# Kernel optimization log

Hardware: AMD Instinct MI355X
Metric: run time of the kernel (lower is better)

Reference implementation:

```python
import jax, jax.numpy as jnp
import numpy as np

N_NODES = 100000
N_EDGES = 600000
IN_DIM, HID_DIM, OUT_DIM = 128, 128, 128
NEG_SLOPE = 0.2  # PyG GATConv default


def _glorot(key, shape):
    fan = sum(shape)
    lim = jnp.sqrt(6.0 / fan)
    return jax.random.uniform(key, shape, jnp.float32, -lim, lim)


def setup_inputs() -> dict:
    key = jax.random.key(0)
    ks = jax.random.split(key, 10)
    x = jax.random.normal(ks[0], (N_NODES, IN_DIM), jnp.float32)
    edge_index = jax.random.randint(ks[1], (2, N_EDGES), 0, N_NODES, jnp.int64)
    return {
        "x": x,
        "edge_index": edge_index,
        "W1": _glorot(ks[2], (IN_DIM, HID_DIM)),
        "a_src1": _glorot(ks[3], (HID_DIM,)),
        "a_dst1": _glorot(ks[4], (HID_DIM,)),
        "b1": jnp.zeros((HID_DIM,), jnp.float32),
        "W2": _glorot(ks[5], (HID_DIM, OUT_DIM)),
        "a_src2": _glorot(ks[6], (OUT_DIM,)),
        "a_dst2": _glorot(ks[7], (OUT_DIM,)),
        "b2": jnp.zeros((OUT_DIM,), jnp.float32),
    }


def _gat_conv(x, src, dst, W, a_src, a_dst, b, n_nodes):
    """Single-head PyG-style GATConv (concat=True, heads=1, with self-loops already in src/dst)."""
    h = x @ W                                   # [N, F]
    alpha_s = h @ a_src                         # [N]
    alpha_d = h @ a_dst                         # [N]
    e = jax.nn.leaky_relu(alpha_s[src] + alpha_d[dst], NEG_SLOPE)  # [E]
    # segment softmax over incoming edges of each dst node
    m = jax.lax.stop_gradient(jax.ops.segment_max(e, dst, num_segments=n_nodes))
    w = jnp.exp(e - m[dst])                     # [E]
    denom = jax.ops.segment_sum(w, dst, num_segments=n_nodes)  # [N]
    alpha = w / denom[dst]                      # [E]
    out = jax.ops.segment_sum(h[src] * alpha[:, None], dst, num_segments=n_nodes)
    return out + b


def reference(x, edge_index, W1, a_src1, a_dst1, b1, W2, a_src2, a_dst2, b2):
    n = x.shape[0]
    loop = jnp.arange(n, dtype=edge_index.dtype)
    src = jnp.concatenate([edge_index[0], loop])  # add self-loops (PyG default)
    dst = jnp.concatenate([edge_index[1], loop])
    h = jax.nn.relu(_gat_conv(x, src, dst, W1, a_src1, a_dst1, b1, n))
    out = _gat_conv(h, src, dst, W2, a_src2, a_dst2, b2, n)
    return out.mean(axis=0)  # [out_dim]
```

## Files before the change

### kernel.cpp

```cpp
#include <hip/hip_runtime.h>


#define NEG_SLOPE 0.2f

typedef __attribute__((ext_vector_type(8))) short bf16x8;
typedef __attribute__((ext_vector_type(4))) float f32x4;

__device__ __forceinline__ float leaky(float x) { return x > 0.0f ? x : NEG_SLOPE * x; }

__device__ __forceinline__ unsigned int bf16rne(float f) {
  unsigned int u = __float_as_uint(f);
  return (u + 0x7fffu + ((u >> 16) & 1u)) >> 16;
}
__device__ __forceinline__ unsigned int packbf(float a, float b) {
  return bf16rne(a) | (bf16rne(b) << 16);
}
__device__ __forceinline__ float bf_lo(unsigned int u) { return __uint_as_float(u << 16); }
__device__ __forceinline__ float bf_hi(unsigned int u) { return __uint_as_float(u & 0xffff0000u); }

__device__ __forceinline__ void accum8(float* a, float w, uint4 h) {
  a[0] += w * bf_lo(h.x); a[1] += w * bf_hi(h.x);
  a[2] += w * bf_lo(h.y); a[3] += w * bf_hi(h.y);
  a[4] += w * bf_lo(h.z); a[5] += w * bf_hi(h.z);
  a[6] += w * bf_lo(h.w); a[7] += w * bf_hi(h.w);
}

__device__ __forceinline__ float gat_node_agg(const uint4* __restrict__ H4,
                                              const float* __restrict__ vas,
                                              const int* __restrict__ esrc,
                                              int s, int deg, float adv, float eself,
                                              uint4 hs, int lane, int l, float* acc) {
  float wself, dsum;
  if (deg <= 16) {
    const bool a = l < deg;
    int uj = 0;
    if (a) uj = esrc[s + l];
    float vsr = vas[uj];
    uint4 hb[8];
#pragma unroll
    for (int i = 0; i < 8; i++) {
      int ut = __shfl(uj, (lane & 48) + i, 64);
      hb[i] = H4[(size_t)ut * 16 + l];
    }
    const bool big = deg > 8;
    uint4 hc[8];
    if (big) {
#pragma unroll
      for (int i = 0; i < 8; i++) {
        int ut = __shfl(uj, (lane & 48) + 8 + i, 64);
        hc[i] = H4[(size_t)ut * 16 + l];
      }
    }
    float wj = a ? __expf(leaky(vsr + adv) - eself) : 0.f;
    wself = 1.0f;
    dsum = wj;
#pragma unroll
    for (int o = 8; o; o >>= 1) dsum += __shfl_xor(dsum, o, 16);
#pragma unroll
    for (int i = 0; i < 8; i++) {
      float w = __shfl(wj, (lane & 48) + i, 64);
      accum8(acc, w, hb[i]);
    }
    if (big) {
#pragma unroll
      for (int i = 0; i < 8; i++) {
        float w = __shfl(wj, (lane & 48) + 8 + i, 64);
        accum8(acc, w, hc[i]);
      }
    }
  } else {
    float m = eself;
    for (int t0 = 0; t0 < deg; t0 += 16) {
      int j = t0 + l;
      if (j < deg) m = fmaxf(m, leaky(vas[esrc[s + j]] + adv));
    }
#pragma unroll
    for (int o = 8; o; o >>= 1) m = fmaxf(m, __shfl_xor(m, o, 16));
    wself = __expf(eself - m);
    float dl = 0.f;
    for (int t0 = 0; t0 < deg; t0 += 16) {
      int j = t0 + l;
      int u2 = 0;
      float w2 = 0.f;
      if (j < deg) {
        u2 = esrc[s + j];
        w2 = __expf(leaky(vas[u2] + adv) - m);
        dl += w2;
      }
      const int cnt = min(16, deg - t0);
      for (int i0 = 0; i0 < cnt; i0 += 8) {
        const int tb = cnt - i0;
        uint4 hb[8];
        float wt[8];
#pragma unroll
        for (int i = 0; i < 8; i++) {
          if (i < tb) {
            int ut = __shfl(u2, (lane & 48) + i0 + i, 64);
            wt[i] = __shfl(w2, (lane & 48) + i0 + i, 64);
            hb[i] = H4[(size_t)ut * 16 + l];
          }
        }
#pragma unroll
        for (int i = 0; i < 8; i++)
          if (i < tb) accum8(acc, wt[i], hb[i]);
      }
    }
    dsum = dl;
#pragma unroll
    for (int o = 8; o; o >>= 1) dsum += __shfl_xor(dsum, o, 16);
  }
  accum8(acc, wself, hs);
  return 1.0f / (dsum + wself);
}

__global__ __launch_bounds__(256) void setup_k(const float* __restrict__ W1,
                                               const float* __restrict__ W2,
                                               unsigned short* __restrict__ Wf1,
                                               unsigned short* __restrict__ Wf2,
                                               int* __restrict__ deg,
                                               float* __restrict__ partial,
                                               int n, int nzb) {
  const int b = blockIdx.x;
  if (b < 2) {
    const float* W = b ? W2 : W1;
    unsigned short* Wf = b ? Wf2 : Wf1;
    for (int idx = threadIdx.x; idx < 16384; idx += 256) {
      int j = idx & 7;
      int lane = (idx >> 3) & 63;
      int fid = idx >> 9;
      int ct = fid >> 2, ks = fid & 3;
      int q = lane >> 4, l15 = lane & 15;
      Wf[idx] = (unsigned short)bf16rne(W[(ks * 32 + q * 8 + j) * 128 + ct * 16 + l15]);
    }
    return;
  }
  if (b == 2) {
    for (int i = threadIdx.x; i < 64 * 128; i += 256) partial[i] = 0.f;
    return;
  }
  int base = (b - 3) * 1024 + threadIdx.x * 4;
#pragma unroll
  for (int i = 0; i < 4; i++)
    if (base + i < n) deg[base + i] = 0;
}

__global__ void hist_kernel(const int* __restrict__ dst, int* __restrict__ deg, int E) {
  int e = blockIdx.x * 256 + threadIdx.x;
  if (e < E) atomicAdd(&deg[dst[e]], 1);
}

__global__ void scan_a(const int* __restrict__ cnt, int* __restrict__ exc,
                       int* __restrict__ bsum, int n) {
  __shared__ int sh[256];
  int b = blockIdx.x, tid = threadIdx.x;
  int base = b * 1024 + tid * 4;
  int v[4];
#pragma unroll
  for (int i = 0; i < 4; i++) v[i] = (base + i < n) ? cnt[base + i] : 0;
  int tsum = v[0] + v[1] + v[2] + v[3];
  sh[tid] = tsum;
  __syncthreads();
  for (int o = 1; o < 256; o <<= 1) {
    int t = (tid >= o) ? sh[tid - o] : 0;
    __syncthreads();
    sh[tid] += t;
    __syncthreads();
  }
  if (tid == 255) bsum[b] = sh[255];
  int run = sh[tid] - tsum;
#pragma unroll
  for (int i = 0; i < 4; i++) {
    if (base + i < n) exc[base + i] = run;
    run += v[i];
  }
}

__global__ void scan_c2(const int* __restrict__ exc, const int* __restrict__ bsum,
                        int* __restrict__ rowst, int* __restrict__ fill, int n, int E,
                        int nb) {
  __shared__ int red[256];
  int b = blockIdx.x, tid = threadIdx.x;
  red[tid] = (tid < b && tid < nb) ? bsum[tid] : 0;
  __syncthreads();
#pragma unroll
  for (int o = 128; o; o >>= 1) {
    if (tid < o) red[tid] += red[tid + o];
    __syncthreads();
  }
  int off = red[0];
  int base = b * 1024 + tid * 4;
#pragma unroll
  for (int i = 0; i < 4; i++) {
    int idx = base + i;
    if (idx < n) {
      int v = exc[idx] + off;
      rowst[idx] = v;
      fill[idx] = v;
    }
  }
  if (b == 0 && tid == 0) rowst[n] = E;
}

__global__ void scatter_kernel(const int* __restrict__ src, const int* __restrict__ dst,
                               int* __restrict__ fill, int* __restrict__ esrc, int E) {
  int e = blockIdx.x * 256 + threadIdx.x;
  if (e < E) {
    int v = dst[e];
    int p = atomicAdd(&fill[v], 1);
    esrc[p] = src[e];
  }
}

__device__ __forceinline__ void cvt_f32(const float4* raw, bf16x8* xf) {
#pragma unroll
  for (int ks = 0; ks < 4; ks++) {
    union { bf16x8 v; unsigned int u[4]; } cv;
    cv.u[0] = packbf(raw[2 * ks].x, raw[2 * ks].y);
    cv.u[1] = packbf(raw[2 * ks].z, raw[2 * ks].w);
    cv.u[2] = packbf(raw[2 * ks + 1].x, raw[2 * ks + 1].y);
    cv.u[3] = packbf(raw[2 * ks + 1].z, raw[2 * ks + 1].w);
    xf[ks] = cv.v;
  }
}

__device__ __forceinline__ void mfma_tile(const unsigned short* WL, const bf16x8* xf,
                                          const float* __restrict__ a_s,
                                          const float* __restrict__ a_d,
                                          unsigned short* __restrict__ H,
                                          float* __restrict__ vas,
                                          float* __restrict__ vad, int myrow, bool act,
                                          int lane, int q) {
  f32x4 acc[8];
#pragma unroll
  for (int ct = 0; ct < 8; ct++) acc[ct] = (f32x4){0.f, 0.f, 0.f, 0.f};
#pragma unroll
  for (int ks = 0; ks < 4; ks++) {
    bf16x8 wf[8];
#pragma unroll
    for (int ct = 0; ct < 8; ct++)
      wf[ct] = *(const bf16x8*)&WL[(((ct << 2) + ks) << 9) + lane * 8];
#pragma unroll
    for (int ct = 0; ct < 8; ct++)
      acc[ct] = __builtin_amdgcn_mfma_f32_16x16x32_bf16(wf[ct], xf[ks], acc[ct], 0, 0, 0);
  }
  float ds = 0.f, dd = 0.f;
#pragma unroll
  for (int ct = 0; ct < 8; ct++) {
    const int c0 = ct * 16 + q * 4;
    float4 as4 = *(const float4*)&a_s[c0];
    float4 ad4 = *(const float4*)&a_d[c0];
    ds += acc[ct][0] * as4.x + acc[ct][1] * as4.y + acc[ct][2] * as4.z + acc[ct][3] * as4.w;
    dd += acc[ct][0] * ad4.x + acc[ct][1] * ad4.y + acc[ct][2] * ad4.z + acc[ct][3] * ad4.w;
    if (act) {
      uint2 o;
      o.x = packbf(acc[ct][0], acc[ct][1]);
      o.y = packbf(acc[ct][2], acc[ct][3]);
      *(uint2*)&H[(size_t)myrow * 128 + c0] = o;
    }
  }
  ds += __shfl_xor(ds, 16, 64);
  ds += __shfl_xor(ds, 32, 64);
  dd += __shfl_xor(dd, 16, 64);
  dd += __shfl_xor(dd, 32, 64);
  if (q == 0 && act) {
    vas[myrow] = ds;
    vad[myrow] = dd;
  }
}

__global__ __launch_bounds__(256) void gemm_mfma1(const float* __restrict__ Xf,
                                                  const unsigned short* __restrict__ Wf,
                                                  const float* __restrict__ a_s,
                                                  const float* __restrict__ a_d,
                                                  unsigned short* __restrict__ H,
                                                  float* __restrict__ vas,
                                                  float* __restrict__ vad, int n,
                                                  int nt16, int ngemm) {
  __shared__ unsigned short WL[32 * 512];
  const int lane = threadIdx.x & 63;
  const int wv = threadIdx.x >> 6;
  const int l15 = lane & 15;
  const int q = lane >> 4;
  const int t0 = blockIdx.x * 4 + wv;
  const int t1 = t0 + ngemm * 4;
  const int r0 = t0 * 16 + l15;
  const int r1 = t1 * 16 + l15;
  const bool wact0 = t0 < nt16;
  const bool wact1 = t1 < nt16;
  const bool act0 = wact0 && (r0 < n);
  const bool act1 = wact1 && (r1 < n);

  float4 raw0[8];
  if (wact0) {
#pragma unroll
    for (int ks = 0; ks < 4; ks++) {
      float4 z = {0.f, 0.f, 0.f, 0.f};
      raw0[2 * ks] = z;
      raw0[2 * ks + 1] = z;
      if (act0) {
        raw0[2 * ks] = *(const float4*)&Xf[(size_t)r0 * 128 + ks * 32 + q * 8];
        raw0[2 * ks + 1] = *(const float4*)&Xf[(size_t)r0 * 128 + ks * 32 + q * 8 + 4];
      }
    }
  }
  {
    const uint4* __restrict__ Wg4 = (const uint4*)Wf;
    uint4* WL4 = (uint4*)WL;
#pragma unroll
    for (int j = 0; j < 8; j++) WL4[threadIdx.x + 256 * j] = Wg4[threadIdx.x + 256 * j];
  }
  __syncthreads();
  if (!wact0) return;

  float4 raw1[8];
  if (wact1) {
#pragma unroll
    for (int ks = 0; ks < 4; ks++) {
      float4 z = {0.f, 0.f, 0.f, 0.f};
      raw1[2 * ks] = z;
      raw1[2 * ks + 1] = z;
      if (act1) {
        raw1[2 * ks] = *(const float4*)&Xf[(size_t)r1 * 128 + ks * 32 + q * 8];
        raw1[2 * ks + 1] = *(const float4*)&Xf[(size_t)r1 * 128 + ks * 32 + q * 8 + 4];
      }
    }
  }

  bf16x8 xf[4];
  cvt_f32(raw0, xf);
  mfma_tile(WL, xf, a_s, a_d, H, vas, vad, r0, act0, lane, q);
  if (wact1) {
    cvt_f32(raw1, xf);
    mfma_tile(WL, xf, a_s, a_d, H, vas, vad, r1, act1, lane, q);
  }
}

__global__ __launch_bounds__(256, 4) void agg1_gemm2(
    const unsigned short* __restrict__ HA, const float* __restrict__ vas1,
    const float* __restrict__ vad1, const int* __restrict__ rowst,
    const int* __restrict__ esrc, const float* __restrict__ b1,
    const unsigned short* __restrict__ Wf2, const float* __restrict__ a_s2,
    const float* __restrict__ a_d2, unsigned short* __restrict__ HB,
    float* __restrict__ vas2, float* __restrict__ vad2, int n) {
  __shared__ unsigned short Atile[16 * 128];
  __shared__ float sdot[2][4][16];
  const int tid = threadIdx.x;
  const int lane = tid & 63;
  const int wv = tid >> 6;
  const int q = lane >> 4;
  const int l = lane & 15;
  const int row = wv * 4 + q;
  const int node = blockIdx.x * 16 + row;
  const uint4* __restrict__ H4 = (const uint4*)HA;

  float acc[8];
#pragma unroll
  for (int k = 0; k < 8; k++) acc[k] = 0.f;

  uint4 o = {0u, 0u, 0u, 0u};
  if (node < n) {
    const int s = rowst[node];
    const int deg = rowst[node + 1] - s;
    const float adv = vad1[node];
    const float eself = leaky(vas1[node] + adv);
    uint4 hs = H4[(size_t)node * 16 + l];
    const float inv = gat_node_agg(H4, vas1, esrc, s, deg, adv, eself, hs, lane, l, acc);

    float4 b0 = *(const float4*)&b1[8 * l];
    float4 b1v = *(const float4*)&b1[8 * l + 4];
    acc[0] = fmaxf(acc[0] * inv + b0.x, 0.f);
    acc[1] = fmaxf(acc[1] * inv + b0.y, 0.f);
    acc[2] = fmaxf(acc[2] * inv + b0.z, 0.f);
    acc[3] = fmaxf(acc[3] * inv + b0.w, 0.f);
    acc[4] = fmaxf(acc[4] * inv + b1v.x, 0.f);
    acc[5] = fmaxf(acc[5] * inv + b1v.y, 0.f);
    acc[6] = fmaxf(acc[6] * inv + b1v.z, 0.f);
    acc[7] = fmaxf(acc[7] * inv + b1v.w, 0.f);
    o.x = packbf(acc[0], acc[1]);
    o.y = packbf(acc[2], acc[3]);
    o.z = packbf(acc[4], acc[5]);
    o.w = packbf(acc[6], acc[7]);
  }
  *(uint4*)&Atile[row * 128 + ((l ^ (row & 7)) << 3)] = o;
  __syncthreads();

  bf16x8 xf[4];
#pragma unroll
  for (int ks = 0; ks < 4; ks++)
    xf[ks] = *(const bf16x8*)&Atile[l * 128 + ((((ks << 2) + q) ^ (l & 7)) << 3)];

  const int ct0 = 2 * wv, ct1 = 2 * wv + 1;
  f32x4 accA = {0.f, 0.f, 0.f, 0.f}, accB = {0.f, 0.f, 0.f, 0.f};
#pragma unroll
  for (int ks = 0; ks < 4; ks++) {
    bf16x8 w0 = *(const bf16x8*)&Wf2[(((ct0 << 2) + ks) << 9) + lane * 8];
    bf16x8 w1 = *(const bf16x8*)&Wf2[(((ct1 << 2) + ks) << 9) + lane * 8];
    accA = __builtin_amdgcn_mfma_f32_16x16x32_bf16(w0, xf[ks], accA, 0, 0, 0);
    accB = __builtin_amdgcn_mfma_f32_16x16x32_bf16(w1, xf[ks], accB, 0, 0, 0);
  }

  const int myrow = blockIdx.x * 16 + l;
  const bool ract = myrow < n;
  float ds = 0.f, dd = 0.f;
  {
    const int c0 = ct0 * 16 + q * 4;
    float4 as4 = *(const float4*)&a_s2[c0];
    float4 ad4 = *(const float4*)&a_d2[c0];
    ds += accA[0] * as4.x + accA[1] * as4.y + accA[2] * as4.z + accA[3] * as4.w;
    dd += accA[0] * ad4.x + accA[1] * ad4.y + accA[2] * ad4.z + accA[3] * ad4.w;
    if (ract) {
      uint2 ov;
      ov.x = packbf(accA[0], accA[1]);
      ov.y = packbf(accA[2], accA[3]);
      *(uint2*)&HB[(size_t)myrow * 128 + c0] = ov;
    }
  }
  {
    const int c0 = ct1 * 16 + q * 4;
    float4 as4 = *(const float4*)&a_s2[c0];
    float4 ad4 = *(const float4*)&a_d2[c0];
    ds += accB[0] * as4.x + accB[1] * as4.y + accB[2] * as4.z + accB[3] * as4.w;
    dd += accB[0] * ad4.x + accB[1] * ad4.y + accB[2] * ad4.z + accB[3] * ad4.w;
    if (ract) {
      uint2 ov;
      ov.x = packbf(accB[0], accB[1]);
      ov.y = packbf(accB[2], accB[3]);
      *(uint2*)&HB[(size_t)myrow * 128 + c0] = ov;
    }
  }
  ds += __shfl_xor(ds, 16, 64);
  ds += __shfl_xor(ds, 32, 64);
  dd += __shfl_xor(dd, 16, 64);
  dd += __shfl_xor(dd, 32, 64);
  if (q == 0) {
    sdot[0][wv][l] = ds;
    sdot[1][wv][l] = dd;
  }
  __syncthreads();
  if (tid < 16) {
    int nn = blockIdx.x * 16 + tid;
    if (nn < n) {
      vas2[nn] = sdot[0][0][tid] + sdot[0][1][tid] + sdot[0][2][tid] + sdot[0][3][tid];
      vad2[nn] = sdot[1][0][tid] + sdot[1][1][tid] + sdot[1][2][tid] + sdot[1][3][tid];
    }
  }
}

__global__ __launch_bounds__(256, 4) void gat_agg_l2(const unsigned short* __restrict__ H,
                                                     const float* __restrict__ vas,
                                                     const float* __restrict__ vad,
                                                     const int* __restrict__ rowst,
                                                     const int* __restrict__ esrc,
                                                     const float* __restrict__ bias,
                                                     float* __restrict__ partial, int n) {
  const int tid = threadIdx.x;
  const int lane = tid & 63;
  const int wv = tid >> 6;
  const int q = lane >> 4;
  const int l = lane & 15;
  const int node = (blockIdx.x * 4 + wv) * 4 + q;
  const uint4* __restrict__ H4 = (const uint4*)H;

  float acc[8];
#pragma unroll
  for (int k = 0; k < 8; k++) acc[k] = 0.f;

  if (node < n) {
    const int s = rowst[node];
    const int deg = rowst[node + 1] - s;
    const float adv = vad[node];
    const float eself = leaky(vas[node] + adv);
    uint4 hs = H4[(size_t)node * 16 + l];
    const float inv = gat_node_agg(H4, vas, esrc, s, deg, adv, eself, hs, lane, l, acc);

    float4 b0 = *(const float4*)&bias[8 * l];
    float4 b1v = *(const float4*)&bias[8 * l + 4];
    acc[0] = acc[0] * inv + b0.x; acc[1] = acc[1] * inv + b0.y;
    acc[2] = acc[2] * inv + b0.z; acc[3] = acc[3] * inv + b0.w;
    acc[4] = acc[4] * inv + b1v.x; acc[5] = acc[5] * inv + b1v.y;
    acc[6] = acc[6] * inv + b1v.z; acc[7] = acc[7] * inv + b1v.w;
  }

#pragma unroll
  for (int k = 0; k < 8; k++) {
    acc[k] += __shfl_xor(acc[k], 16, 64);
    acc[k] += __shfl_xor(acc[k], 32, 64);
  }
  __shared__ float red[4][128];
  if (q == 0) {
#pragma unroll
    for (int k = 0; k < 8; k++) red[wv][8 * l + k] = acc[k];
  }
  __syncthreads();
  if (tid < 128) {
    float sm = red[0][tid] + red[1][tid] + red[2][tid] + red[3][tid];
    atomicAdd(&partial[(blockIdx.x & 63) * 128 + tid], sm);
  }
}

__global__ void finalize_k(const float* __restrict__ partial, float* __restrict__ out,
                           float invn) {
  int c = threadIdx.x;
  float s = 0.f;
#pragma unroll 8
  for (int r = 0; r < 64; r++) s += partial[r * 128 + c];
  out[c] = s * invn;
}

extern "C" void kernel_launch(void* const* d_in, const int* in_sizes, int n_in,
                              void* d_out, int out_size, void* d_ws, size_t ws_size,
                              hipStream_t stream) {
  const float* x = (const float*)d_in[0];
  const int* ei = (const int*)d_in[1];
  const float* W1 = (const float*)d_in[2];
  const float* a_src1 = (const float*)d_in[3];
  const float* a_dst1 = (const float*)d_in[4];
  const float* b1 = (const float*)d_in[5];
  const float* W2 = (const float*)d_in[6];
  const float* a_src2 = (const float*)d_in[7];
  const float* a_dst2 = (const float*)d_in[8];
  const float* b2 = (const float*)d_in[9];
  float* out = (float*)d_out;

  const int N = in_sizes[0] / 128;
  const int E = in_sizes[1] / 2;
  const int* src = ei;
  const int* dst = ei + E;

  const size_t rowpadded = (size_t)(N + 256) * 128;

  char* p = (char*)d_ws;
  unsigned short* HA = (unsigned short*)p; p += rowpadded * 2;
  unsigned short* HB = (unsigned short*)p; p += rowpadded * 2;
  float* vas1 = (float*)p;    p += (size_t)N * 4;
  float* vad1 = (float*)p;    p += (size_t)N * 4;
  float* vas2 = (float*)p;    p += (size_t)N * 4;
  float* vad2 = (float*)p;    p += (size_t)N * 4;
  int* deg = (int*)p;         p += (size_t)N * 4;
  int* rowst = (int*)p;       p += (size_t)(N + 1) * 4;
  int* fill = (int*)p;        p += (size_t)N * 4;
  int* esrc = (int*)p;        p += (size_t)E * 4;
  int* exc = (int*)p;         p += (size_t)N * 4;
  int* bsum = (int*)p;        p += 256 * 4;
  float* partial = (float*)p; p += 64 * 128 * 4;
  unsigned short* Wf1 = (unsigned short*)p; p += 16384 * 2;
  unsigned short* Wf2 = (unsigned short*)p; p += 16384 * 2;

  const int nb = (N + 1023) / 1024;
  const int eblocks = (E + 255) / 256;
  const int nt16 = (N + 15) / 16;
  const int ngemm = (nt16 + 7) / 8;
  const int aggblocks = (N + 15) / 16;

  setup_k<<<3 + nb, 256, 0, stream>>>(W1, W2, Wf1, Wf2, deg, partial, N, nb);
  hist_kernel<<<eblocks, 256, 0, stream>>>(dst, deg, E);
  scan_a<<<nb, 256, 0, stream>>>(deg, exc, bsum, N);
  scan_c2<<<nb, 256, 0, stream>>>(exc, bsum, rowst, fill, N, E, nb);
  scatter_kernel<<<eblocks, 256, 0, stream>>>(src, dst, fill, esrc, E);
  gemm_mfma1<<<ngemm, 256, 0, stream>>>(x, Wf1, a_src1, a_dst1, HA, vas1, vad1, N, nt16, ngemm);
  agg1_gemm2<<<aggblocks, 256, 0, stream>>>(HA, vas1, vad1, rowst, esrc, b1, Wf2,
                                            a_src2, a_dst2, HB, vas2, vad2, N);
  gat_agg_l2<<<aggblocks, 256, 0, stream>>>(HB, vas2, vad2, rowst, esrc, b2, partial, N);
  finalize_k<<<1, 128, 0, stream>>>(partial, out, 1.0f / (float)N);
}
```

Before: 267.7 us.

## Add padded per-node 16-slot neighbor table to cut dependent loads in aggregation

```diff
diff --git a/kernel.cpp b/kernel.cpp
--- a/kernel.cpp
+++ b/kernel.cpp
@@ -27,27 +27,32 @@
 
 __device__ __forceinline__ float gat_node_agg(const uint4* __restrict__ H4,
                                               const float* __restrict__ vas,
+                                              const int* __restrict__ dega,
+                                              const int* __restrict__ esrcp,
+                                              const int* __restrict__ rowst,
                                               const int* __restrict__ esrc,
-                                              int s, int deg, float adv, float eself,
-                                              uint4 hs, int lane, int l, float* acc) {
+                                              int node, int nclamp, float adv,
+                                              float eself, uint4 hs, int lane, int l,
+                                              float* acc) {
+  int traw = esrcp[(size_t)node * 16 + l];
+  int dg = dega[node];
+  int ujc = min(max(traw, 0), nclamp);
+  float vsr = vas[ujc];
+  uint4 hb[8];
+#pragma unroll
+  for (int i = 0; i < 8; i++) {
+    int ut = __shfl(ujc, (lane & 48) + i, 64);
+    hb[i] = H4[(size_t)ut * 16 + l];
+  }
   float wself, dsum;
-  if (deg <= 16) {
-    const bool a = l < deg;
-    int uj = 0;
-    if (a) uj = esrc[s + l];
-    float vsr = vas[uj];
-    uint4 hb[8];
-#pragma unroll
-    for (int i = 0; i < 8; i++) {
-      int ut = __shfl(uj, (lane & 48) + i, 64);
-      hb[i] = H4[(size_t)ut * 16 + l];
-    }
-    const bool big = deg > 8;
+  if (dg <= 16) {
+    const bool a = l < dg;
+    const bool big = dg > 8;
     uint4 hc[8];
     if (big) {
 #pragma unroll
       for (int i = 0; i < 8; i++) {
-        int ut = __shfl(uj, (lane & 48) + 8 + i, 64);
+        int ut = __shfl(ujc, (lane & 48) + 8 + i, 64);
         hc[i] = H4[(size_t)ut * 16 + l];
       }
     }
@@ -69,6 +74,8 @@
       }
     }
   } else {
+    const int s = rowst[node];
+    const int deg = dg;
     float m = eself;
     for (int t0 = 0; t0 < deg; t0 += 16) {
       int j = t0 + l;
@@ -90,19 +97,19 @@
       const int cnt = min(16, deg - t0);
       for (int i0 = 0; i0 < cnt; i0 += 8) {
         const int tb = cnt - i0;
-        uint4 hb[8];
+        uint4 h2[8];
         float wt[8];
 #pragma unroll
         for (int i = 0; i < 8; i++) {
           if (i < tb) {
             int ut = __shfl(u2, (lane & 48) + i0 + i, 64);
             wt[i] = __shfl(w2, (lane & 48) + i0 + i, 64);
-            hb[i] = H4[(size_t)ut * 16 + l];
+            h2[i] = H4[(size_t)ut * 16 + l];
           }
         }
 #pragma unroll
         for (int i = 0; i < 8; i++)
-          if (i < tb) accum8(acc, wt[i], hb[i]);
+          if (i < tb) accum8(acc, wt[i], h2[i]);
       }
     }
     dsum = dl;
@@ -202,12 +209,16 @@
 }
 
 __global__ void scatter_kernel(const int* __restrict__ src, const int* __restrict__ dst,
-                               int* __restrict__ fill, int* __restrict__ esrc, int E) {
+                               int* __restrict__ fill, const int* __restrict__ rowst,
+                               int* __restrict__ esrc, int* __restrict__ esrcp, int E) {
   int e = blockIdx.x * 256 + threadIdx.x;
   if (e < E) {
     int v = dst[e];
+    int sv = src[e];
     int p = atomicAdd(&fill[v], 1);
-    esrc[p] = src[e];
+    esrc[p] = sv;
+    int p2 = p - rowst[v];
+    if (p2 < 16) esrcp[(size_t)v * 16 + p2] = sv;
   }
 }
 
@@ -337,7 +348,8 @@
 
 __global__ __launch_bounds__(256, 4) void agg1_gemm2(
     const unsigned short* __restrict__ HA, const float* __restrict__ vas1,
-    const float* __restrict__ vad1, const int* __restrict__ rowst,
+    const float* __restrict__ vad1, const int* __restrict__ dega,
+    const int* __restrict__ esrcp, const int* __restrict__ rowst,
     const int* __restrict__ esrc, const float* __restrict__ b1,
     const unsigned short* __restrict__ Wf2, const float* __restrict__ a_s2,
     const float* __restrict__ a_d2, unsigned short* __restrict__ HB,
@@ -359,12 +371,12 @@
 
   uint4 o = {0u, 0u, 0u, 0u};
   if (node < n) {
-    const int s = rowst[node];
-    const int deg = rowst[node + 1] - s;
     const float adv = vad1[node];
-    const float eself = leaky(vas1[node] + adv);
+    const float vsn = vas1[node];
     uint4 hs = H4[(size_t)node * 16 + l];
-    const float inv = gat_node_agg(H4, vas1, esrc, s, deg, adv, eself, hs, lane, l, acc);
+    const float eself = leaky(vsn + adv);
+    const float inv = gat_node_agg(H4, vas1, dega, esrcp, rowst, esrc, node, n - 1,
+                                   adv, eself, hs, lane, l, acc);
 
     float4 b0 = *(const float4*)&b1[8 * l];
     float4 b1v = *(const float4*)&b1[8 * l + 4];
@@ -449,6 +461,8 @@
 __global__ __launch_bounds__(256, 4) void gat_agg_l2(const unsigned short* __restrict__ H,
                                                      const float* __restrict__ vas,
                                                      const float* __restrict__ vad,
+                                                     const int* __restrict__ dega,
+                                                     const int* __restrict__ esrcp,
                                                      const int* __restrict__ rowst,
                                                      const int* __restrict__ esrc,
                                                      const float* __restrict__ bias,
@@ -466,12 +480,12 @@
   for (int k = 0; k < 8; k++) acc[k] = 0.f;
 
   if (node < n) {
-    const int s = rowst[node];
-    const int deg = rowst[node + 1] - s;
     const float adv = vad[node];
-    const float eself = leaky(vas[node] + adv);
+    const float vsn = vas[node];
     uint4 hs = H4[(size_t)node * 16 + l];
-    const float inv = gat_node_agg(H4, vas, esrc, s, deg, adv, eself, hs, lane, l, acc);
+    const float eself = leaky(vsn + adv);
+    const float inv = gat_node_agg(H4, vas, dega, esrcp, rowst, esrc, node, n - 1,
+                                   adv, eself, hs, lane, l, acc);
 
     float4 b0 = *(const float4*)&bias[8 * l];
     float4 b1v = *(const float4*)&bias[8 * l + 4];
@@ -540,6 +554,7 @@
   int* rowst = (int*)p;       p += (size_t)(N + 1) * 4;
   int* fill = (int*)p;        p += (size_t)N * 4;
   int* esrc = (int*)p;        p += (size_t)E * 4;
+  int* esrcp = (int*)p;       p += (size_t)N * 16 * 4;
   int* exc = (int*)p;         p += (size_t)N * 4;
   int* bsum = (int*)p;        p += 256 * 4;
   float* partial = (float*)p; p += 64 * 128 * 4;
@@ -556,10 +571,11 @@
   hist_kernel<<<eblocks, 256, 0, stream>>>(dst, deg, E);
   scan_a<<<nb, 256, 0, stream>>>(deg, exc, bsum, N);
   scan_c2<<<nb, 256, 0, stream>>>(exc, bsum, rowst, fill, N, E, nb);
-  scatter_kernel<<<eblocks, 256, 0, stream>>>(src, dst, fill, esrc, E);
+  scatter_kernel<<<eblocks, 256, 0, stream>>>(src, dst, fill, rowst, esrc, esrcp, E);
   gemm_mfma1<<<ngemm, 256, 0, stream>>>(x, Wf1, a_src1, a_dst1, HA, vas1, vad1, N, nt16, ngemm);
-  agg1_gemm2<<<aggblocks, 256, 0, stream>>>(HA, vas1, vad1, rowst, esrc, b1, Wf2,
-                                            a_src2, a_dst2, HB, vas2, vad2, N);
-  gat_agg_l2<<<aggblocks, 256, 0, stream>>>(HB, vas2, vad2, rowst, esrc, b2, partial, N);
+  agg1_gemm2<<<aggblocks, 256, 0, stream>>>(HA, vas1, vad1, deg, esrcp, rowst, esrc, b1,
+                                            Wf2, a_src2, a_dst2, HB, vas2, vad2, N);
+  gat_agg_l2<<<aggblocks, 256, 0, stream>>>(HB, vas2, vad2, deg, esrcp, rowst, esrc, b2,
+                                            partial, N);
   finalize_k<<<1, 128, 0, stream>>>(partial, out, 1.0f / (float)N);
 }
```

Result: no change. 270.6 us (+1.1%).

## Replace CSR build with padded 16-slot adjacency plus overflow list, two nodes per group

Applied to the files above, without the earlier changes.

```diff
diff --git a/kernel.cpp b/kernel.cpp
--- a/kernel.cpp
+++ b/kernel.cpp
@@ -25,101 +25,116 @@
   a[6] += w * bf_lo(h.w); a[7] += w * bf_hi(h.w);
 }
 
-__device__ __forceinline__ float gat_node_agg(const uint4* __restrict__ H4,
-                                              const float* __restrict__ vas,
-                                              const int* __restrict__ esrc,
-                                              int s, int deg, float adv, float eself,
-                                              uint4 hs, int lane, int l, float* acc) {
-  float wself, dsum;
-  if (deg <= 16) {
-    const bool a = l < deg;
-    int uj = 0;
-    if (a) uj = esrc[s + l];
-    float vsr = vas[uj];
-    uint4 hb[8];
+__device__ __forceinline__ float2 gat_node2(
+    const uint4* __restrict__ H4, const float* __restrict__ vas,
+    const float* __restrict__ vad, const int* __restrict__ fill,
+    const int* __restrict__ esrcp, const int2* __restrict__ ovf,
+    const int* __restrict__ ovfn, int node0, int node1, int nclamp,
+    int lane, int l, float* acc0, float* acc1, float* eself_out) {
+  int t0 = esrcp[(size_t)node0 * 16 + l];
+  int t1 = esrcp[(size_t)node1 * 16 + l];
+  int dg0 = fill[node0];
+  int dg1 = fill[node1];
+  float ad0 = vad[node0], ad1 = vad[node1];
+  float as0 = vas[node0], as1 = vas[node1];
+  uint4 hs0 = H4[(size_t)node0 * 16 + l];
+  uint4 hs1 = H4[(size_t)node1 * 16 + l];
+  int u0 = min(max(t0, 0), nclamp);
+  int u1 = min(max(t1, 0), nclamp);
+  float vs0 = vas[u0];
+  float vs1 = vas[u1];
+  uint4 hb0[8], hb1[8];
+#pragma unroll
+  for (int i = 0; i < 8; i++) {
+    int ut = __shfl(u0, (lane & 48) + i, 64);
+    hb0[i] = H4[(size_t)ut * 16 + l];
+  }
+#pragma unroll
+  for (int i = 0; i < 8; i++) {
+    int ut = __shfl(u1, (lane & 48) + i, 64);
+    hb1[i] = H4[(size_t)ut * 16 + l];
+  }
+  const bool big0 = dg0 > 8, big1 = dg1 > 8;
+  uint4 hc0[8];
+  if (big0) {
 #pragma unroll
     for (int i = 0; i < 8; i++) {
-      int ut = __shfl(uj, (lane & 48) + i, 64);
-      hb[i] = H4[(size_t)ut * 16 + l];
-    }
-    const bool big = deg > 8;
-    uint4 hc[8];
-    if (big) {
-#pragma unroll
-      for (int i = 0; i < 8; i++) {
-        int ut = __shfl(uj, (lane & 48) + 8 + i, 64);
-        hc[i] = H4[(size_t)ut * 16 + l];
+      int ut = __shfl(u0, (lane & 48) + 8 + i, 64);
+      hc0[i] = H4[(size_t)ut * 16 + l];
+    }
+  }
+  float es0 = leaky(as0 + ad0), es1 = leaky(as1 + ad1);
+  float wj0 = (l < dg0) ? __expf(leaky(vs0 + ad0) - es0) : 0.f;
+  float wj1 = (l < dg1) ? __expf(leaky(vs1 + ad1) - es1) : 0.f;
+  float ds0 = wj0, ds1 = wj1;
+#pragma unroll
+  for (int o = 8; o; o >>= 1) ds0 += __shfl_xor(ds0, o, 16);
+#pragma unroll
+  for (int o = 8; o; o >>= 1) ds1 += __shfl_xor(ds1, o, 16);
+#pragma unroll
+  for (int i = 0; i < 8; i++) {
+    float w = __shfl(wj0, (lane & 48) + i, 64);
+    accum8(acc0, w, hb0[i]);
+  }
+  if (big0) {
+#pragma unroll
+    for (int i = 0; i < 8; i++) {
+      float w = __shfl(wj0, (lane & 48) + 8 + i, 64);
+      accum8(acc0, w, hc0[i]);
+    }
+  }
+  uint4 hc1[8];
+  if (big1) {
+#pragma unroll
+    for (int i = 0; i < 8; i++) {
+      int ut = __shfl(u1, (lane & 48) + 8 + i, 64);
+      hc1[i] = H4[(size_t)ut * 16 + l];
+    }
+  }
+#pragma unroll
+  for (int i = 0; i < 8; i++) {
+    float w = __shfl(wj1, (lane & 48) + i, 64);
+    accum8(acc1, w, hb1[i]);
+  }
+  if (big1) {
+#pragma unroll
+    for (int i = 0; i < 8; i++) {
+      float w = __shfl(wj1, (lane & 48) + 8 + i, 64);
+      accum8(acc1, w, hc1[i]);
+    }
+  }
+  if (dg0 > 16 || dg1 > 16) {
+    int ovn = *ovfn;
+    for (int k = 0; k < ovn; k++) {
+      int2 ent = ovf[k];
+      if (ent.x == node0) {
+        float w = __expf(leaky(vas[ent.y] + ad0) - es0);
+        ds0 += w;
+        accum8(acc0, w, H4[(size_t)ent.y * 16 + l]);
       }
-    }
-    float wj = a ? __expf(leaky(vsr + adv) - eself) : 0.f;
-    wself = 1.0f;
-    dsum = wj;
-#pragma unroll
-    for (int o = 8; o; o >>= 1) dsum += __shfl_xor(dsum, o, 16);
-#pragma unroll
-    for (int i = 0; i < 8; i++) {
-      float w = __shfl(wj, (lane & 48) + i, 64);
-      accum8(acc, w, hb[i]);
-    }
-    if (big) {
-#pragma unroll
-      for (int i = 0; i < 8; i++) {
-        float w = __shfl(wj, (lane & 48) + 8 + i, 64);
-        accum8(acc, w, hc[i]);
+      if (ent.x == node1) {
+        float w = __expf(leaky(vas[ent.y] + ad1) - es1);
+        ds1 += w;
+        accum8(acc1, w, H4[(size_t)ent.y * 16 + l]);
       }
     }
-  } else {
-    float m = eself;
-    for (int t0 = 0; t0 < deg; t0 += 16) {
-      int j = t0 + l;
-      if (j < deg) m = fmaxf(m, leaky(vas[esrc[s + j]] + adv));
-    }
-#pragma unroll
-    for (int o = 8; o; o >>= 1) m = fmaxf(m, __shfl_xor(m, o, 16));
-    wself = __expf(eself - m);
-    float dl = 0.f;
-    for (int t0 = 0; t0 < deg; t0 += 16) {
-      int j = t0 + l;
-      int u2 = 0;
-      float w2 = 0.f;
-      if (j < deg) {
-        u2 = esrc[s + j];
-        w2 = __expf(leaky(vas[u2] + adv) - m);
-        dl += w2;
-      }
-      const int cnt = min(16, deg - t0);
-      for (int i0 = 0; i0 < cnt; i0 += 8) {
-        const int tb = cnt - i0;
-        uint4 hb[8];
-        float wt[8];
-#pragma unroll
-        for (int i = 0; i < 8; i++) {
-          if (i < tb) {
-            int ut = __shfl(u2, (lane & 48) + i0 + i, 64);
-            wt[i] = __shfl(w2, (lane & 48) + i0 + i, 64);
-            hb[i] = H4[(size_t)ut * 16 + l];
-          }
-        }
-#pragma unroll
-        for (int i = 0; i < 8; i++)
-          if (i < tb) accum8(acc, wt[i], hb[i]);
-      }
-    }
-    dsum = dl;
-#pragma unroll
-    for (int o = 8; o; o >>= 1) dsum += __shfl_xor(dsum, o, 16);
-  }
-  accum8(acc, wself, hs);
-  return 1.0f / (dsum + wself);
+  }
+  accum8(acc0, 1.0f, hs0);
+  accum8(acc1, 1.0f, hs1);
+  eself_out[0] = es0;
+  eself_out[1] = es1;
+  return make_float2(1.0f / (ds0 + 1.0f), 1.0f / (ds1 + 1.0f));
 }
 
 __global__ __launch_bounds__(256) void setup_k(const float* __restrict__ W1,
                                                const float* __restrict__ W2,
                                                unsigned short* __restrict__ Wf1,
                                                unsigned short* __restrict__ Wf2,
-                                               int* __restrict__ deg,
+                                               int* __restrict__ fill,
+                                               int* __restrict__ esrcp,
+                                               int* __restrict__ ovfn,
                                                float* __restrict__ partial,
-                                               int n, int nzb) {
+                                               int n, int nfb) {
   const int b = blockIdx.x;
   if (b < 2) {
     const float* W = b ? W2 : W1;
@@ -136,78 +151,39 @@
   }
   if (b == 2) {
     for (int i = threadIdx.x; i < 64 * 128; i += 256) partial[i] = 0.f;
+    if (threadIdx.x == 0) *ovfn = 0;
     return;
   }
-  int base = (b - 3) * 1024 + threadIdx.x * 4;
-#pragma unroll
-  for (int i = 0; i < 4; i++)
-    if (base + i < n) deg[base + i] = 0;
-}
-
-__global__ void hist_kernel(const int* __restrict__ dst, int* __restrict__ deg, int E) {
-  int e = blockIdx.x * 256 + threadIdx.x;
-  if (e < E) atomicAdd(&deg[dst[e]], 1);
-}
-
-__global__ void scan_a(const int* __restrict__ cnt, int* __restrict__ exc,
-                       int* __restrict__ bsum, int n) {
-  __shared__ int sh[256];
-  int b = blockIdx.x, tid = threadIdx.x;
-  int base = b * 1024 + tid * 4;
-  int v[4];
-#pragma unroll
-  for (int i = 0; i < 4; i++) v[i] = (base + i < n) ? cnt[base + i] : 0;
-  int tsum = v[0] + v[1] + v[2] + v[3];
-  sh[tid] = tsum;
-  __syncthreads();
-  for (int o = 1; o < 256; o <<= 1) {
-    int t = (tid >= o) ? sh[tid - o] : 0;
-    __syncthreads();
-    sh[tid] += t;
-    __syncthreads();
-  }
-  if (tid == 255) bsum[b] = sh[255];
-  int run = sh[tid] - tsum;
-#pragma unroll
-  for (int i = 0; i < 4; i++) {
-    if (base + i < n) exc[base + i] = run;
-    run += v[i];
-  }
-}
-
-__global__ void scan_c2(const int* __restrict__ exc, const int* __restrict__ bsum,
-                        int* __restrict__ rowst, int* __restrict__ fill, int n, int E,
-                        int nb) {
-  __shared__ int red[256];
-  int b = blockIdx.x, tid = threadIdx.x;
-  red[tid] = (tid < b && tid < nb) ? bsum[tid] : 0;
-  __syncthreads();
-#pragma unroll
-  for (int o = 128; o; o >>= 1) {
-    if (tid < o) red[tid] += red[tid + o];
-    __syncthreads();
-  }
-  int off = red[0];
-  int base = b * 1024 + tid * 4;
-#pragma unroll
-  for (int i = 0; i < 4; i++) {
-    int idx = base + i;
-    if (idx < n) {
-      int v = exc[idx] + off;
-      rowst[idx] = v;
-      fill[idx] = v;
-    }
-  }
-  if (b == 0 && tid == 0) rowst[n] = E;
+  if (b < 3 + nfb) {
+    int base = (b - 3) * 1024 + threadIdx.x * 4;
+#pragma unroll
+    for (int i = 0; i < 4; i++)
+      if (base + i < n) fill[base + i] = 0;
+    return;
+  }
+  size_t base = (size_t)(b - 3 - nfb) * 1024 + threadIdx.x * 4;
+  size_t tot = (size_t)n * 16;
+  if (base + 4 <= tot) {
+    *(int4*)&esrcp[base] = make_int4(0, 0, 0, 0);
+  } else {
+    for (size_t i = base; i < tot; i++) esrcp[i] = 0;
+  }
 }
 
 __global__ void scatter_kernel(const int* __restrict__ src, const int* __restrict__ dst,
-                               int* __restrict__ fill, int* __restrict__ esrc, int E) {
+                               int* __restrict__ fill, int* __restrict__ esrcp,
+                               int2* __restrict__ ovf, int* __restrict__ ovfn, int E) {
   int e = blockIdx.x * 256 + threadIdx.x;
   if (e < E) {
     int v = dst[e];
+    int sv = src[e];
     int p = atomicAdd(&fill[v], 1);
-    esrc[p] = src[e];
+    if (p < 16) {
+      esrcp[(size_t)v * 16 + p] = sv;
+    } else {
+      int k = atomicAdd(ovfn, 1);
+      ovf[k] = make_int2(v, sv);
+    }
   }
 }
 
@@ -335,161 +311,178 @@
   }
 }
 
-__global__ __launch_bounds__(256, 4) void agg1_gemm2(
+__global__ __launch_bounds__(256, 3) void agg1_gemm2(
     const unsigned short* __restrict__ HA, const float* __restrict__ vas1,
-    const float* __restrict__ vad1, const int* __restrict__ rowst,
-    const int* __restrict__ esrc, const float* __restrict__ b1,
+    const float* __restrict__ vad1, const int* __restrict__ fill,
+    const int* __restrict__ esrcp, const int2* __restrict__ ovf,
+    const int* __restrict__ ovfn, const float* __restrict__ b1,
     const unsigned short* __restrict__ Wf2, const float* __restrict__ a_s2,
     const float* __restrict__ a_d2, unsigned short* __restrict__ HB,
     float* __restrict__ vas2, float* __restrict__ vad2, int n) {
-  __shared__ unsigned short Atile[16 * 128];
-  __shared__ float sdot[2][4][16];
+  __shared__ unsigned short Atile[32 * 128];
+  __shared__ float sdot[2][2][4][16];
   const int tid = threadIdx.x;
   const int lane = tid & 63;
   const int wv = tid >> 6;
   const int q = lane >> 4;
   const int l = lane & 15;
   const int row = wv * 4 + q;
-  const int node = blockIdx.x * 16 + row;
+  const int base = blockIdx.x * 32;
+  const int node0 = base + row;
+  const int node1 = base + row + 16;
+  const bool valid0 = node0 < n, valid1 = node1 < n;
+  const int n0s = valid0 ? node0 : n - 1;
+  const int n1s = valid1 ? node1 : n - 1;
   const uint4* __restrict__ H4 = (const uint4*)HA;
 
-  float acc[8];
-#pragma unroll
-  for (int k = 0; k < 8; k++) acc[k] = 0.f;
-
-  uint4 o = {0u, 0u, 0u, 0u};
-  if (node < n) {
-    const int s = rowst[node];
-    const int deg = rowst[node + 1] - s;
-    const float adv = vad1[node];
-    const float eself = leaky(vas1[node] + adv);
-    uint4 hs = H4[(size_t)node * 16 + l];
-    const float inv = gat_node_agg(H4, vas1, esrc, s, deg, adv, eself, hs, lane, l, acc);
-
-    float4 b0 = *(const float4*)&b1[8 * l];
-    float4 b1v = *(const float4*)&b1[8 * l + 4];
-    acc[0] = fmaxf(acc[0] * inv + b0.x, 0.f);
-    acc[1] = fmaxf(acc[1] * inv + b0.y, 0.f);
-    acc[2] = fmaxf(acc[2] * inv + b0.z, 0.f);
-    acc[3] = fmaxf(acc[3] * inv + b0.w, 0.f);
-    acc[4] = fmaxf(acc[4] * inv + b1v.x, 0.f);
-    acc[5] = fmaxf(acc[5] * inv + b1v.y, 0.f);
-    acc[6] = fmaxf(acc[6] * inv + b1v.z, 0.f);
-    acc[7] = fmaxf(acc[7] * inv + b1v.w, 0.f);
-    o.x = packbf(acc[0], acc[1]);
-    o.y = packbf(acc[2], acc[3]);
-    o.z = packbf(acc[4], acc[5]);
-    o.w = packbf(acc[6], acc[7]);
-  }
-  *(uint4*)&Atile[row * 128 + ((l ^ (row & 7)) << 3)] = o;
+  float acc0[8], acc1[8];
+#pragma unroll
+  for (int k = 0; k < 8; k++) { acc0[k] = 0.f; acc1[k] = 0.f; }
+  float es[2];
+  float2 inv = gat_node2(H4, vas1, vad1, fill, esrcp, ovf, ovfn, n0s, n1s, n - 1,
+                         lane, l, acc0, acc1, es);
+
+  float4 b0 = *(const float4*)&b1[8 * l];
+  float4 b1v = *(const float4*)&b1[8 * l + 4];
+  uint4 o0 = {0u, 0u, 0u, 0u}, o1 = {0u, 0u, 0u, 0u};
+  if (valid0) {
+    float r0_ = fmaxf(acc0[0] * inv.x + b0.x, 0.f), r1_ = fmaxf(acc0[1] * inv.x + b0.y, 0.f);
+    float r2_ = fmaxf(acc0[2] * inv.x + b0.z, 0.f), r3_ = fmaxf(acc0[3] * inv.x + b0.w, 0.f);
+    float r4_ = fmaxf(acc0[4] * inv.x + b1v.x, 0.f), r5_ = fmaxf(acc0[5] * inv.x + b1v.y, 0.f);
+    float r6_ = fmaxf(acc0[6] * inv.x + b1v.z, 0.f), r7_ = fmaxf(acc0[7] * inv.x + b1v.w, 0.f);
+    o0.x = packbf(r0_, r1_); o0.y = packbf(r2_, r3_);
+    o0.z = packbf(r4_, r5_); o0.w = packbf(r6_, r7_);
+  }
+  if (valid1) {
+    float r0_ = fmaxf(acc1[0] * inv.y + b0.x, 0.f), r1_ = fmaxf(acc1[1] * inv.y + b0.y, 0.f);
+    float r2_ = fmaxf(acc1[2] * inv.y + b0.z, 0.f), r3_ = fmaxf(acc1[3] * inv.y + b0.w, 0.f);
+    float r4_ = fmaxf(acc1[4] * inv.y + b1v.x, 0.f), r5_ = fmaxf(acc1[5] * inv.y + b1v.y, 0.f);
+    float r6_ = fmaxf(acc1[6] * inv.y + b1v.z, 0.f), r7_ = fmaxf(acc1[7] * inv.y + b1v.w, 0.f);
+    o1.x = packbf(r0_, r1_); o1.y = packbf(r2_, r3_);
+    o1.z = packbf(r4_, r5_); o1.w = packbf(r6_, r7_);
+  }
+  *(uint4*)&Atile[row * 128 + ((l ^ (row & 7)) << 3)] = o0;
+  *(uint4*)&Atile[(row + 16) * 128 + ((l ^ (row & 7)) << 3)] = o1;
   __syncthreads();
 
-  bf16x8 xf[4];
-#pragma unroll
-  for (int ks = 0; ks < 4; ks++)
-    xf[ks] = *(const bf16x8*)&Atile[l * 128 + ((((ks << 2) + q) ^ (l & 7)) << 3)];
-
   const int ct0 = 2 * wv, ct1 = 2 * wv + 1;
-  f32x4 accA = {0.f, 0.f, 0.f, 0.f}, accB = {0.f, 0.f, 0.f, 0.f};
+  f32x4 aA0 = {0.f, 0.f, 0.f, 0.f}, aB0 = aA0, aA1 = aA0, aB1 = aA0;
 #pragma unroll
   for (int ks = 0; ks < 4; ks++) {
     bf16x8 w0 = *(const bf16x8*)&Wf2[(((ct0 << 2) + ks) << 9) + lane * 8];
     bf16x8 w1 = *(const bf16x8*)&Wf2[(((ct1 << 2) + ks) << 9) + lane * 8];
-    accA = __builtin_amdgcn_mfma_f32_16x16x32_bf16(w0, xf[ks], accA, 0, 0, 0);
-    accB = __builtin_amdgcn_mfma_f32_16x16x32_bf16(w1, xf[ks], accB, 0, 0, 0);
-  }
-
-  const int myrow = blockIdx.x * 16 + l;
-  const bool ract = myrow < n;
-  float ds = 0.f, dd = 0.f;
-  {
-    const int c0 = ct0 * 16 + q * 4;
-    float4 as4 = *(const float4*)&a_s2[c0];
-    float4 ad4 = *(const float4*)&a_d2[c0];
-    ds += accA[0] * as4.x + accA[1] * as4.y + accA[2] * as4.z + accA[3] * as4.w;
-    dd += accA[0] * ad4.x + accA[1] * ad4.y + accA[2] * ad4.z + accA[3] * ad4.w;
-    if (ract) {
-      uint2 ov;
-      ov.x = packbf(accA[0], accA[1]);
-      ov.y = packbf(accA[2], accA[3]);
-      *(uint2*)&HB[(size_t)myrow * 128 + c0] = ov;
-    }
-  }
-  {
-    const int c0 = ct1 * 16 + q * 4;
-    float4 as4 = *(const float4*)&a_s2[c0];
-    float4 ad4 = *(const float4*)&a_d2[c0];
-    ds += accB[0] * as4.x + accB[1] * as4.y + accB[2] * as4.z + accB[3] * as4.w;
-    dd += accB[0] * ad4.x + accB[1] * ad4.y + accB[2] * ad4.z + accB[3] * ad4.w;
-    if (ract) {
-      uint2 ov;
-      ov.x = packbf(accB[0], accB[1]);
-      ov.y = packbf(accB[2], accB[3]);
-      *(uint2*)&HB[(size_t)myrow * 128 + c0] = ov;
-    }
-  }
-  ds += __shfl_xor(ds, 16, 64);
-  ds += __shfl_xor(ds, 32, 64);
-  dd += __shfl_xor(dd, 16, 64);
-  dd += __shfl_xor(dd, 32, 64);
-  if (q == 0) {
-    sdot[0][wv][l] = ds;
-    sdot[1][wv][l] = dd;
+    bf16x8 x0 = *(const bf16x8*)&Atile[l * 128 + ((((ks << 2) + q) ^ (l & 7)) << 3)];
+    bf16x8 x1 = *(const bf16x8*)&Atile[(16 + l) * 128 + ((((ks << 2) + q) ^ (l & 7)) << 3)];
+    aA0 = __builtin_amdgcn_mfma_f32_16x16x32_bf16(w0, x0, aA0, 0, 0, 0);
+    aB0 = __builtin_amdgcn_mfma_f32_16x16x32_bf16(w1, x0, aB0, 0, 0, 0);
+    aA1 = __builtin_amdgcn_mfma_f32_16x16x32_bf16(w0, x1, aA1, 0, 0, 0);
+    aB1 = __builtin_amdgcn_mfma_f32_16x16x32_bf16(w1, x1, aB1, 0, 0, 0);
+  }
+
+#pragma unroll
+  for (int t = 0; t < 2; t++) {
+    f32x4 aA = t ? aA1 : aA0;
+    f32x4 aB = t ? aB1 : aB0;
+    const int myrow = base + t * 16 + l;
+    const bool ract = myrow < n;
+    float ds = 0.f, dd = 0.f;
+    {
+      const int c0 = ct0 * 16 + q * 4;
+      float4 as4 = *(const float4*)&a_s2[c0];
+      float4 ad4 = *(const float4*)&a_d2[c0];
+      ds += aA[0] * as4.x + aA[1] * as4.y + aA[2] * as4.z + aA[3] * as4.w;
+      dd += aA[0] * ad4.x + aA[1] * ad4.y + aA[2] * ad4.z + aA[3] * ad4.w;
+      if (ract) {
+        uint2 ov;
+        ov.x = packbf(aA[0], aA[1]);
+        ov.y = packbf(aA[2], aA[3]);
+        *(uint2*)&HB[(size_t)myrow * 128 + c0] = ov;
+      }
+    }
+    {
+      const int c0 = ct1 * 16 + q * 4;
+      float4 as4 = *(const float4*)&a_s2[c0];
+      float4 ad4 = *(const float4*)&a_d2[c0];
+      ds += aB[0] * as4.x + aB[1] * as4.y + aB[2] * as4.z + aB[3] * as4.w;
+      dd += aB[0] * ad4.x + aB[1] * ad4.y + aB[2] * ad4.z + aB[3] * ad4.w;
+      if (ract) {
+        uint2 ov;
+        ov.x = packbf(aB[0], aB[1]);
+        ov.y = packbf(aB[2], aB[3]);
+        *(uint2*)&HB[(size_t)myrow * 128 + c0] = ov;
+      }
+    }
+    ds += __shfl_xor(ds, 16, 64);
+    ds += __shfl_xor(ds, 32, 64);
+    dd += __shfl_xor(dd, 16, 64);
+    dd += __shfl_xor(dd, 32, 64);
+    if (q == 0) {
+      sdot[t][0][wv][l] = ds;
+      sdot[t][1][wv][l] = dd;
+    }
   }
   __syncthreads();
-  if (tid < 16) {
-    int nn = blockIdx.x * 16 + tid;
+  if (tid < 32) {
+    int t = tid >> 4, i = tid & 15;
+    int nn = base + tid;
     if (nn < n) {
-      vas2[nn] = sdot[0][0][tid] + sdot[0][1][tid] + sdot[0][2][tid] + sdot[0][3][tid];
-      vad2[nn] = sdot[1][0][tid] + sdot[1][1][tid] + sdot[1][2][tid] + sdot[1][3][tid];
-    }
-  }
-}
-
-__global__ __launch_bounds__(256, 4) void gat_agg_l2(const unsigned short* __restrict__ H,
-                                                     const float* __restrict__ vas,
-                                                     const float* __restrict__ vad,
-                                                     const int* __restrict__ rowst,
-                                                     const int* __restrict__ esrc,
-                                                     const float* __restrict__ bias,
-                                                     float* __restrict__ partial, int n) {
+      vas2[nn] = sdot[t][0][0][i] + sdot[t][0][1][i] + sdot[t][0][2][i] + sdot[t][0][3][i];
+      vad2[nn] = sdot[t][1][0][i] + sdot[t][1][1][i] + sdot[t][1][2][i] + sdot[t][1][3][i];
+    }
+  }
+}
+
+__global__ __launch_bounds__(256, 3) void gat_agg_l2(
+    const unsigned short* __restrict__ H, const float* __restrict__ vas,
+    const float* __restrict__ vad, const int* __restrict__ fill,
+    const int* __restrict__ esrcp, const int2* __restrict__ ovf,
+    const int* __restrict__ ovfn, const float* __restrict__ bias,
+    float* __restrict__ partial, int n) {
   const int tid = threadIdx.x;
   const int lane = tid & 63;
   const int wv = tid >> 6;
   const int q = lane >> 4;
   const int l = lane & 15;
-  const int node = (blockIdx.x * 4 + wv) * 4 + q;
+  const int row = wv * 4 + q;
+  const int base = blockIdx.x * 32;
+  const int node0 = base + row;
+  const int node1 = base + row + 16;
+  const bool valid0 = node0 < n, valid1 = node1 < n;
+  const int n0s = valid0 ? node0 : n - 1;
+  const int n1s = valid1 ? node1 : n - 1;
   const uint4* __restrict__ H4 = (const uint4*)H;
 
-  float acc[8];
-#pragma unroll
-  for (int k = 0; k < 8; k++) acc[k] = 0.f;
-
-  if (node < n) {
-    const int s = rowst[node];
-    const int deg = rowst[node + 1] - s;
-    const float adv = vad[node];
-    const float eself = leaky(vas[node] + adv);
-    uint4 hs = H4[(size_t)node * 16 + l];
-    const float inv = gat_node_agg(H4, vas, esrc, s, deg, adv, eself, hs, lane, l, acc);
-
-    float4 b0 = *(const float4*)&bias[8 * l];
-    float4 b1v = *(const float4*)&bias[8 * l + 4];
-    acc[0] = acc[0] * inv + b0.x; acc[1] = acc[1] * inv + b0.y;
-    acc[2] = acc[2] * inv + b0.z; acc[3] = acc[3] * inv + b0.w;
-    acc[4] = acc[4] * inv + b1v.x; acc[5] = acc[5] * inv + b1v.y;
-    acc[6] = acc[6] * inv + b1v.z; acc[7] = acc[7] * inv + b1v.w;
-  }
+  float acc0[8], acc1[8];
+#pragma unroll
+  for (int k = 0; k < 8; k++) { acc0[k] = 0.f; acc1[k] = 0.f; }
+  float es[2];
+  float2 inv = gat_node2(H4, vas, vad, fill, esrcp, ovf, ovfn, n0s, n1s, n - 1,
+                         lane, l, acc0, acc1, es);
+
+  float4 b0 = *(const float4*)&bias[8 * l];
+  float4 b1v = *(const float4*)&bias[8 * l + 4];
+  float out[8];
+  const float i0 = valid0 ? inv.x : 0.f;
+  const float i1 = valid1 ? inv.y : 0.f;
+  const float bm = (valid0 ? 1.f : 0.f) + (valid1 ? 1.f : 0.f);
+  out[0] = acc0[0] * i0 + acc1[0] * i1 + bm * b0.x;
+  out[1] = acc0[1] * i0 + acc1[1] * i1 + bm * b0.y;
+  out[2] = acc0[2] * i0 + acc1[2] * i1 + bm * b0.z;
+  out[3] = acc0[3] * i0 + acc1[3] * i1 + bm * b0.w;
+  out[4] = acc0[4] * i0 + acc1[4] * i1 + bm * b1v.x;
+  out[5] = acc0[5] * i0 + acc1[5] * i1 + bm * b1v.y;
+  out[6] = acc0[6] * i0 + acc1[6] * i1 + bm * b1v.z;
+  out[7] = acc0[7] * i0 + acc1[7] * i1 + bm * b1v.w;
 
 #pragma unroll
   for (int k = 0; k < 8; k++) {
-    acc[k] += __shfl_xor(acc[k], 16, 64);
-    acc[k] += __shfl_xor(acc[k], 32, 64);
+    out[k] += __shfl_xor(out[k], 16, 64);
+    out[k] += __shfl_xor(out[k], 32, 64);
   }
   __shared__ float red[4][128];
   if (q == 0) {
 #pragma unroll
-    for (int k = 0; k < 8; k++) red[wv][8 * l + k] = acc[k];
+    for (int k = 0; k < 8; k++) red[wv][8 * l + k] = out[k];
   }
   __syncthreads();
   if (tid < 128) {
@@ -536,30 +529,28 @@
   float* vad1 = (float*)p;    p += (size_t)N * 4;
   float* vas2 = (float*)p;    p += (size_t)N * 4;
   float* vad2 = (float*)p;    p += (size_t)N * 4;
-  int* deg = (int*)p;         p += (size_t)N * 4;
-  int* rowst = (int*)p;       p += (size_t)(N + 1) * 4;
   int* fill = (int*)p;        p += (size_t)N * 4;
-  int* esrc = (int*)p;        p += (size_t)E * 4;
-  int* exc = (int*)p;         p += (size_t)N * 4;
-  int* bsum = (int*)p;        p += 256 * 4;
+  int* esrcp = (int*)p;       p += (size_t)N * 16 * 4;
+  int2* ovf = (int2*)p;       p += (size_t)E * 8;
+  int* ovfn = (int*)p;        p += 16;
   float* partial = (float*)p; p += 64 * 128 * 4;
   unsigned short* Wf1 = (unsigned short*)p; p += 16384 * 2;
   unsigned short* Wf2 = (unsigned short*)p; p += 16384 * 2;
 
-  const int nb = (N + 1023) / 1024;
   const int eblocks = (E + 255) / 256;
   const int nt16 = (N + 15) / 16;
   const int ngemm = (nt16 + 7) / 8;
-  const int aggblocks = (N + 15) / 16;
-
-  setup_k<<<3 + nb, 256, 0, stream>>>(W1, W2, Wf1, Wf2, deg, partial, N, nb);
-  hist_kernel<<<eblocks, 256, 0, stream>>>(dst, deg, E);
-  scan_a<<<nb, 256, 0, stream>>>(deg, exc, bsum, N);
-  scan_c2<<<nb, 256, 0, stream>>>(exc, bsum, rowst, fill, N, E, nb);
-  scatter_kernel<<<eblocks, 256, 0, stream>>>(src, dst, fill, esrc, E);
+  const int aggblocks = (N + 31) / 32;
+  const int nfb = (N + 1023) / 1024;
+  const int neb = (N * 16 + 1023) / 1024;
+
+  setup_k<<<3 + nfb + neb, 256, 0, stream>>>(W1, W2, Wf1, Wf2, fill, esrcp, ovfn,
+                                             partial, N, nfb);
+  scatter_kernel<<<eblocks, 256, 0, stream>>>(src, dst, fill, esrcp, ovf, ovfn, E);
   gemm_mfma1<<<ngemm, 256, 0, stream>>>(x, Wf1, a_src1, a_dst1, HA, vas1, vad1, N, nt16, ngemm);
-  agg1_gemm2<<<aggblocks, 256, 0, stream>>>(HA, vas1, vad1, rowst, esrc, b1, Wf2,
-                                            a_src2, a_dst2, HB, vas2, vad2, N);
-  gat_agg_l2<<<aggblocks, 256, 0, stream>>>(HB, vas2, vad2, rowst, esrc, b2, partial, N);
+  agg1_gemm2<<<aggblocks, 256, 0, stream>>>(HA, vas1, vad1, fill, esrcp, ovf, ovfn, b1,
+                                            Wf2, a_src2, a_dst2, HB, vas2, vad2, N);
+  gat_agg_l2<<<aggblocks, 256, 0, stream>>>(HB, vas2, vad2, fill, esrcp, ovf, ovfn, b2,
+                                            partial, N);
   finalize_k<<<1, 128, 0, stream>>>(partial, out, 1.0f / (float)N);
 }
```

New measurement: 232.8 us. 1.15x faster.
